# Kernel optimization log

Hardware: AMD Instinct MI355X
Metric: run time of the kernel (lower is better)

Reference implementation:

```python
import jax, jax.numpy as jnp
import numpy as np

B, C, D, H, W = 1, 128, 8, 32, 32
NH, HD = 8, 16            # num_heads, head_dim = C // NH
PD, PH, PW = 2, 4, 4      # local patch dims
RD, RH, RW = 2, 2, 2      # global K/V reduction ratios
MLPH = 4 * C              # mlp_ratio = 4
EPS = 1e-5
SCALE = HD ** -0.5


def setup_inputs() -> dict:
    key = jax.random.key(0)
    ks = iter(jax.random.split(key, 16))
    def w(shape, scale=0.02):
        return jax.random.normal(next(ks), shape, jnp.float32) * scale
    inp = {"x": jax.random.normal(next(ks), (B, C, D, H, W), jnp.float32)}
    for p in ("l", "g"):  # local branch / global branch transformer blocks
        inp[f"{p}_n1_g"] = jnp.ones((C,), jnp.float32)
        inp[f"{p}_n1_b"] = jnp.zeros((C,), jnp.float32)
        inp[f"{p}_qkv_w"] = w((3 * C, C))            # Linear(dim, 3*dim, bias=False)
        inp[f"{p}_proj_w"] = w((C, C))
        inp[f"{p}_proj_b"] = jnp.zeros((C,), jnp.float32)
        inp[f"{p}_n2_g"] = jnp.ones((C,), jnp.float32)
        inp[f"{p}_n2_b"] = jnp.zeros((C,), jnp.float32)
        inp[f"{p}_fc1_w"] = w((MLPH, C))
        inp[f"{p}_fc1_b"] = jnp.zeros((MLPH,), jnp.float32)
        inp[f"{p}_fc2_w"] = w((C, MLPH))
        inp[f"{p}_fc2_b"] = jnp.zeros((C,), jnp.float32)
    inp["g_ke_w"] = w((C, C, RD, RH, RW))  # Conv3d(dim, dim, k=stride=(2,2,2), bias=False)
    inp["g_ve_w"] = w((C, C, RD, RH, RW))
    inp["g_nk_g"] = jnp.ones((HD,), jnp.float32)
    inp["g_nk_b"] = jnp.zeros((HD,), jnp.float32)
    inp["g_nv_g"] = jnp.ones((HD,), jnp.float32)
    inp["g_nv_b"] = jnp.zeros((HD,), jnp.float32)
    return inp


def _ln(t, g, b):
    m = t.mean(-1, keepdims=True)
    v = jnp.square(t - m).mean(-1, keepdims=True)
    return (t - m) * jax.lax.rsqrt(v + EPS) * g + b


def _mlp(t, w1, b1, w2, b2):
    return jax.nn.gelu(t @ w1.T + b1, approximate=False) @ w2.T + b2


def _forward(x, l_n1_g, l_n1_b, l_qkv_w, l_proj_w, l_proj_b, l_n2_g, l_n2_b,
             l_fc1_w, l_fc1_b, l_fc2_w, l_fc2_b,
             g_n1_g, g_n1_b, g_qkv_w, g_ke_w, g_ve_w, g_nk_g, g_nk_b,
             g_nv_g, g_nv_b, g_proj_w, g_proj_b, g_n2_g, g_n2_b,
             g_fc1_w, g_fc1_b, g_fc2_w, g_fc2_b):
    nd, nh, nw = D // PD, H // PH, W // PW
    R, Npl = nd * nh * nw, PD * PH * PW
    N = D * H * W

    # ---------------- Local branch ----------------
    # (B,C,D,H,W) -> (B, R, Npl, C) patch tokens
    loc = x.reshape(B, C, nd, PD, nh, PH, nw, PW)
    loc = loc.transpose(0, 2, 4, 6, 3, 5, 7, 1).reshape(B, R, Npl, C)
    y = _ln(loc, l_n1_g, l_n1_b)
    qkv = (y @ l_qkv_w.T).reshape(B, R, Npl, 3, NH, HD).transpose(3, 0, 1, 4, 2, 5)
    q, k, v = qkv[0], qkv[1], qkv[2]  # (B,R,NH,Npl,HD)
    attn = jax.nn.softmax(jnp.einsum('brhnd,brhmd->brhnm', q, k) * SCALE, axis=-1)
    o = jnp.einsum('brhnm,brhmd->brhnd', attn, v)
    # faithful to torch: (attn@v).transpose(-1,-2).reshape(B,R,Npl,C)
    o = jnp.swapaxes(o, -1, -2).reshape(B, R, Npl, C)
    loc = loc + (o @ l_proj_w.T + l_proj_b)
    loc = loc + _mlp(_ln(loc, l_n2_g, l_n2_b), l_fc1_w, l_fc1_b, l_fc2_w, l_fc2_b)
    # back to (B,C,D,H,W)
    loc_y = loc.reshape(B, nd, nh, nw, PD, PH, PW, C)
    loc_y = loc_y.transpose(0, 7, 1, 4, 2, 5, 3, 6).reshape(B, C, D, H, W)

    # ---------------- Global branch ----------------
    g = x.reshape(B, C, N).transpose(0, 2, 1)  # (B,N,C)
    y = _ln(g, g_n1_g, g_n1_b)
    qkv = y @ g_qkv_w.T  # (B,N,3C)
    q, k, v = jnp.split(qkv, 3, axis=-1)
    qh = q.reshape(B, N, NH, HD).transpose(0, 2, 1, 3)  # (B,NH,N,HD)
    dn = ('NCDHW', 'OIDHW', 'NCDHW')
    def _reduce(t, wc):
        tm = t.transpose(0, 2, 1).reshape(B, C, D, H, W)
        tr = jax.lax.conv_general_dilated(tm, wc, (RD, RH, RW), 'VALID',
                                          dimension_numbers=dn)
        nr = tr.shape[2] * tr.shape[3] * tr.shape[4]
        return tr.reshape(B, C, nr).transpose(0, 2, 1).reshape(B, nr, NH, HD).transpose(0, 2, 1, 3)
    kr = _ln(_reduce(k, g_ke_w), g_nk_g, g_nk_b)  # (B,NH,Nr,HD)
    vr = _ln(_reduce(v, g_ve_w), g_nv_g, g_nv_b)
    attn = jax.nn.softmax(jnp.einsum('bhnd,bhmd->bhnm', qh, kr) * SCALE, axis=-1)
    o = jnp.einsum('bhnm,bhmd->bhnd', attn, vr)
    o = o.transpose(0, 2, 1, 3).reshape(B, N, C)
    g = g + (o @ g_proj_w.T + g_proj_b)
    g = g + _mlp(_ln(g, g_n2_g, g_n2_b), g_fc1_w, g_fc1_b, g_fc2_w, g_fc2_b)
    glo_y = g.transpose(0, 2, 1).reshape(B, C, D, H, W)

    # ---------------- Gate ----------------
    return x * jax.nn.sigmoid(loc_y + glo_y)


def reference(x, l_n1_g, l_n1_b, l_qkv_w, l_proj_w, l_proj_b, l_n2_g, l_n2_b,
              l_fc1_w, l_fc1_b, l_fc2_w, l_fc2_b,
              g_n1_g, g_n1_b, g_qkv_w, g_ke_w, g_ve_w, g_nk_g, g_nk_b,
              g_nv_g, g_nv_b, g_proj_w, g_proj_b, g_n2_g, g_n2_b,
              g_fc1_w, g_fc1_b, g_fc2_w, g_fc2_b):
    return _forward(x, l_n1_g, l_n1_b, l_qkv_w, l_proj_w, l_proj_b, l_n2_g, l_n2_b,
                    l_fc1_w, l_fc1_b, l_fc2_w, l_fc2_b,
                    g_n1_g, g_n1_b, g_qkv_w, g_ke_w, g_ve_w, g_nk_g, g_nk_b,
                    g_nv_g, g_nv_b, g_proj_w, g_proj_b, g_n2_g, g_n2_b,
                    g_fc1_w, g_fc1_b, g_fc2_w, g_fc2_b)
```

## Files before the change

kernel.cpp:

```cpp
#include <hip/hip_runtime.h>
#include <math.h>

#define N_TOK 8192
#define C_DIM 128
#define NHD   8
#define HDIM  16
#define NR    1024
#define EPSV  1e-5f
#define QK_SCALE 0.25f
#define QK_L2E  0.36067376f

typedef __attribute__((ext_vector_type(8))) short short8;
typedef __attribute__((ext_vector_type(4))) float f32x4;

__device__ __forceinline__ float gelu_f(float v) {
    return 0.5f * v * (1.0f + erff(v * 0.70710678118654752f));
}
__device__ __forceinline__ float uaf(unsigned int u) {
    union { unsigned int u; float f; } x; x.u = u; return x.f;
}
__device__ __forceinline__ short f2b(float v) {
    union { float f; unsigned int u; } x; x.f = v;
    unsigned int r = x.u + 0x7fffu + ((x.u >> 16) & 1u);
    return (short)(r >> 16);
}
__device__ __forceinline__ void ld16bf(const short* p, float* d) {
    uint4 a = *(const uint4*)p;
    uint4 b = *(const uint4*)(p + 8);
    d[0]  = uaf(a.x << 16); d[1]  = uaf(a.x & 0xffff0000u);
    d[2]  = uaf(a.y << 16); d[3]  = uaf(a.y & 0xffff0000u);
    d[4]  = uaf(a.z << 16); d[5]  = uaf(a.z & 0xffff0000u);
    d[6]  = uaf(a.w << 16); d[7]  = uaf(a.w & 0xffff0000u);
    d[8]  = uaf(b.x << 16); d[9]  = uaf(b.x & 0xffff0000u);
    d[10] = uaf(b.y << 16); d[11] = uaf(b.y & 0xffff0000u);
    d[12] = uaf(b.z << 16); d[13] = uaf(b.z & 0xffff0000u);
    d[14] = uaf(b.w << 16); d[15] = uaf(b.w & 0xffff0000u);
}

struct CvtDesc { const float* src; short* dst; int n; int pad; };
struct CvtArgs { CvtDesc d[10]; };

__global__ __launch_bounds__(256) void cvtrans_k(const float* __restrict__ x,
                                                 float* __restrict__ xt, CvtArgs ca) {
    __shared__ float tile[32][33];
    int t = threadIdx.x;
    if (blockIdx.x < 1024) {
        int bx = blockIdx.x & 255, by = blockIdx.x >> 8;
        int tx = t & 31, ty = t >> 5;
        int n0 = bx * 32, c0 = by * 32;
#pragma unroll
        for (int k = 0; k < 4; ++k)
            tile[ty + k * 8][tx] = x[(size_t)(c0 + ty + k * 8) * N_TOK + n0 + tx];
        __syncthreads();
#pragma unroll
        for (int k = 0; k < 4; ++k)
            xt[(size_t)(n0 + ty + k * 8) * C_DIM + c0 + tx] = tile[tx][ty + k * 8];
        return;
    }
    int bid = blockIdx.x - 1024;
#pragma unroll 1
    for (int d = 0; d < 10; ++d) {
        CvtDesc dd = ca.d[d];
        if (dd.pad) {
            for (int i = bid * 256 + t; i < dd.n; i += 40 * 256) {
                int co = i >> 10, qq = i & 1023;
                dd.dst[co * 1024 + ((qq & 7) << 7) + (qq >> 3)] = f2b(dd.src[i]);
            }
        } else {
            for (int i = bid * 256 + t; i < dd.n; i += 40 * 256)
                dd.dst[i] = f2b(dd.src[i]);
        }
    }
}

__global__ __launch_bounds__(256) void ln_token_k(const float* __restrict__ in,
                                                  const float* __restrict__ g1, const float* __restrict__ b1,
                                                  short* __restrict__ o1,
                                                  const float* __restrict__ g2, const float* __restrict__ b2,
                                                  short* __restrict__ o2) {
    int lane = threadIdx.x & 63;
    int n = blockIdx.x * 4 + (threadIdx.x >> 6);
    float v0 = in[(size_t)n * C_DIM + lane];
    float v1 = in[(size_t)n * C_DIM + 64 + lane];
    float s = v0 + v1, sq = v0 * v0 + v1 * v1;
#pragma unroll
    for (int off = 32; off >= 1; off >>= 1) {
        s += __shfl_xor(s, off);
        sq += __shfl_xor(sq, off);
    }
    float m = s * (1.0f / 128.0f);
    float var = sq * (1.0f / 128.0f) - m * m;
    float rs = rsqrtf(var + EPSV);
    float h0 = (v0 - m) * rs, h1 = (v1 - m) * rs;
    o1[(size_t)n * C_DIM + lane]      = f2b(h0 * g1[lane] + b1[lane]);
    o1[(size_t)n * C_DIM + 64 + lane] = f2b(h1 * g1[lane + 64] + b1[lane + 64]);
    o2[(size_t)n * C_DIM + lane]      = f2b(h0 * g2[lane] + b2[lane]);
    o2[(size_t)n * C_DIM + 64 + lane] = f2b(h1 * g2[lane + 64] + b2[lane + 64]);
}

__global__ __launch_bounds__(256) void ln2_pair_k(const float* __restrict__ in0,
                                                  const float* __restrict__ g0, const float* __restrict__ b0,
                                                  short* __restrict__ o0,
                                                  const float* __restrict__ in1,
                                                  const float* __restrict__ g1, const float* __restrict__ b1,
                                                  short* __restrict__ o1) {
    int blk = blockIdx.x;
    bool sel = blk >= 2048;
    blk &= 2047;
    const float* in = sel ? in1 : in0;
    const float* g  = sel ? g1 : g0;
    const float* b  = sel ? b1 : b0;
    short* o        = sel ? o1 : o0;
    int lane = threadIdx.x & 63;
    int n = blk * 4 + (threadIdx.x >> 6);
    float v0 = in[(size_t)n * C_DIM + lane];
    float v1 = in[(size_t)n * C_DIM + 64 + lane];
    float s = v0 + v1, sq = v0 * v0 + v1 * v1;
#pragma unroll
    for (int off = 32; off >= 1; off >>= 1) {
        s += __shfl_xor(s, off);
        sq += __shfl_xor(sq, off);
    }
    float m = s * (1.0f / 128.0f);
    float var = sq * (1.0f / 128.0f) - m * m;
    float rs = rsqrtf(var + EPSV);
    o[(size_t)n * C_DIM + lane]      = f2b((v0 - m) * rs * g[lane] + b[lane]);
    o[(size_t)n * C_DIM + 64 + lane] = f2b((v1 - m) * rs * g[lane + 64] + b[lane + 64]);
}

struct MArgs {
    const short* A[2]; const short* W[2];
    const float* bias[2]; const float* res[2];
    void* out[2];
};
template <int EPI>
__global__ __launch_bounds__(256) void mgemm_k(MArgs ga, int M, int N, int K) {
    int zi = blockIdx.z;
    const short* A = ga.A[zi];
    const short* W = ga.W[zi];
    __shared__ short As[128 * 64];
    __shared__ short Bs[128 * 64];
    int t = threadIdx.x;
    int w = t >> 6, l = t & 63;
    int m0 = blockIdx.x * 128, n0 = blockIdx.y * 128;
    int wm = (w >> 1) * 64, wn = (w & 1) * 64;

    f32x4 acc[4][4];
#pragma unroll
    for (int a = 0; a < 4; ++a)
#pragma unroll
        for (int b = 0; b < 4; ++b) acc[a][b] = f32x4{0.f, 0.f, 0.f, 0.f};

    for (int k0 = 0; k0 < K; k0 += 64) {
        __syncthreads();
#pragma unroll
        for (int c = 0; c < 4; ++c) {
            int chunk = c * 256 + t;
            int row = chunk >> 3;
            int slot = chunk & 7;
            int ss = slot ^ (row & 7);
            uint4 av = *(const uint4*)(A + (size_t)(m0 + row) * K + k0 + slot * 8);
            *(uint4*)(As + row * 64 + ss * 8) = av;
            uint4 wv = *(const uint4*)(W + (size_t)(n0 + row) * K + k0 + slot * 8);
            *(uint4*)(Bs + row * 64 + ss * 8) = wv;
        }
        __syncthreads();
#pragma unroll
        for (int kk = 0; kk < 2; ++kk) {
            short8 af[4], bf[4];
            int sl = kk * 4 + (l >> 4);
#pragma unroll
            for (int mf = 0; mf < 4; ++mf) {
                int row = wm + mf * 16 + (l & 15);
                af[mf] = *(const short8*)(As + row * 64 + (sl ^ (row & 7)) * 8);
            }
#pragma unroll
            for (int nf = 0; nf < 4; ++nf) {
                int row = wn + nf * 16 + (l & 15);
                bf[nf] = *(const short8*)(Bs + row * 64 + (sl ^ (row & 7)) * 8);
            }
#pragma unroll
            for (int mf = 0; mf < 4; ++mf)
#pragma unroll
                for (int nf = 0; nf < 4; ++nf)
                    acc[mf][nf] = __builtin_amdgcn_mfma_f32_16x16x32_bf16(
                        af[mf], bf[nf], acc[mf][nf], 0, 0, 0);
        }
    }

#pragma unroll
    for (int mf = 0; mf < 4; ++mf) {
#pragma unroll
        for (int nf = 0; nf < 4; ++nf) {
            int col = n0 + wn + nf * 16 + (l & 15);
#pragma unroll
            for (int j = 0; j < 4; ++j) {
                int row = m0 + wm + mf * 16 + (l >> 4) * 4 + j;
                float v = acc[mf][nf][j];
                if (EPI == 0) {
                    ((short*)ga.out[zi])[(size_t)row * N + col] = f2b(v);
                } else if (EPI == 1) {
                    v += ga.bias[zi][col] + ga.res[zi][(size_t)row * N + col];
                    ((float*)ga.out[zi])[(size_t)row * N + col] = v;
                } else if (EPI == 2) {
                    v = gelu_f(v + ga.bias[zi][col]);
                    ((short*)ga.out[zi])[(size_t)row * N + col] = f2b(v);
                }
            }
        }
    }
}

struct CLArgs {
    const short* qkv_g; const short* wk; const short* wv;
    float* kpart; float* vpart;
    const short* qkv_l; short* ob;
};
__global__ __launch_bounds__(256) void convlat_k(CLArgs ga) {
    __shared__ char smem[32768];
    int t = threadIdx.x;
    if (blockIdx.x < 128) {
        int bid = blockIdx.x;
        int m0 = (bid & 7) * 128;
        int zi = bid >> 6;
        int slice = (bid >> 3) & 7;
        const short* Abase = ga.qkv_g + (zi ? 256 : 128);
        const short* W = zi ? ga.wv : ga.wk;
        float* outp = zi ? ga.vpart : ga.kpart;
        short* As = (short*)smem;
        short* Bs = (short*)smem + 128 * 64;
        int w = t >> 6, l = t & 63;
        int wm = (w >> 1) * 64, wn = (w & 1) * 64;
        int kbeg = slice * 128;

        f32x4 acc[4][4];
#pragma unroll
        for (int a = 0; a < 4; ++a)
#pragma unroll
            for (int b = 0; b < 4; ++b) acc[a][b] = f32x4{0.f, 0.f, 0.f, 0.f};

        for (int k0 = kbeg; k0 < kbeg + 128; k0 += 64) {
            __syncthreads();
            int off = k0 >> 7;
            int od = off >> 2, oh = (off >> 1) & 1, ow = off & 1;
#pragma unroll
            for (int c = 0; c < 4; ++c) {
                int chunk = c * 256 + t;
                int row = chunk >> 3;
                int slot = chunk & 7;
                int ss = slot ^ (row & 7);
                int nr = m0 + row;
                int ci = (k0 & 127) + slot * 8;
                int n = (2 * (nr >> 8) + od) * 1024 + (2 * ((nr >> 4) & 15) + oh) * 32
                        + 2 * (nr & 15) + ow;
                uint4 av = *(const uint4*)(Abase + (size_t)n * 384 + ci);
                *(uint4*)(As + row * 64 + ss * 8) = av;
                uint4 wv2 = *(const uint4*)(W + (size_t)row * 1024 + k0 + slot * 8);
                *(uint4*)(Bs + row * 64 + ss * 8) = wv2;
            }
            __syncthreads();
#pragma unroll
            for (int kk = 0; kk < 2; ++kk) {
                short8 af[4], bf[4];
                int sl = kk * 4 + (l >> 4);
#pragma unroll
                for (int mf = 0; mf < 4; ++mf) {
                    int row = wm + mf * 16 + (l & 15);
                    af[mf] = *(const short8*)(As + row * 64 + (sl ^ (row & 7)) * 8);
                }
#pragma unroll
                for (int nf = 0; nf < 4; ++nf) {
                    int row = wn + nf * 16 + (l & 15);
                    bf[nf] = *(const short8*)(Bs + row * 64 + (sl ^ (row & 7)) * 8);
                }
#pragma unroll
                for (int mf = 0; mf < 4; ++mf)
#pragma unroll
                    for (int nf = 0; nf < 4; ++nf)
                        acc[mf][nf] = __builtin_amdgcn_mfma_f32_16x16x32_bf16(
                            af[mf], bf[nf], acc[mf][nf], 0, 0, 0);
            }
        }
#pragma unroll
        for (int mf = 0; mf < 4; ++mf)
#pragma unroll
            for (int nf = 0; nf < 4; ++nf) {
                int col = wn + nf * 16 + (l & 15);
#pragma unroll
                for (int j = 0; j < 4; ++j) {
                    int row = m0 + wm + mf * 16 + (l >> 4) * 4 + j;
                    outp[(size_t)slice * (NR * C_DIM) + (size_t)row * C_DIM + col] =
                        acc[mf][nf][j];
                }
            }
        return;
    }
    float (*ks)[32][HDIM] = (float(*)[32][HDIM])smem;
    float (*vs)[32][HDIM] = (float(*)[32][HDIM])(smem + 16384);
    int m = t & 31, h = t >> 5, r = blockIdx.x - 128;
    int zd = r >> 6, zh = (r >> 3) & 7, zw = r & 7;
    int pd = m >> 4, ph = (m >> 2) & 3, pw = m & 3;
    int n = (zd * 2 + pd) * 1024 + (zh * 4 + ph) * 32 + (zw * 4 + pw);
    const short* base = ga.qkv_l + (size_t)n * 384 + h * HDIM;
    float q[16], kt[16], vt[16];
    ld16bf(base, q);
    ld16bf(base + 128, kt);
    ld16bf(base + 256, vt);
#pragma unroll
    for (int d = 0; d < 16; ++d) { ks[h][m][d] = kt[d]; vs[h][m][d] = vt[d]; }
    __syncthreads();
    float s[32];
#pragma unroll
    for (int j = 0; j < 32; ++j) {
        float d = 0.f;
#pragma unroll
        for (int dd = 0; dd < 16; ++dd) d += q[dd] * ks[h][j][dd];
        s[j] = __expf(d * QK_SCALE);
    }
    float sum = 0.f;
#pragma unroll
    for (int j = 0; j < 32; ++j) sum += s[j];
    float inv = 1.0f / sum;
    float oo[16] = {};
#pragma unroll
    for (int j = 0; j < 32; ++j) {
        float p = s[j] * inv;
#pragma unroll
        for (int dd = 0; dd < 16; ++dd) oo[dd] += p * vs[h][j][dd];
    }
#pragma unroll
    for (int dd = 0; dd < 16; ++dd) {
        int n2 = h * 4 + (dd >> 2);
        int c2 = (dd & 3) * 32 + m;
        int pd2 = n2 >> 4, ph2 = (n2 >> 2) & 3, pw2 = n2 & 3;
        int nn = (zd * 2 + pd2) * 1024 + (zh * 4 + ph2) * 32 + (zw * 4 + pw2);
        ga.ob[(size_t)nn * C_DIM + c2] = f2b(oo[dd]);
    }
}

__global__ __launch_bounds__(256) void ln_head_sum_k(const float* __restrict__ kpart,
                                                     const float* __restrict__ vpart,
                                                     const float* __restrict__ gk, const float* __restrict__ bk,
                                                     const float* __restrict__ gv, const float* __restrict__ bv,
                                                     short* __restrict__ kout, short* __restrict__ vout) {
    int idx = blockIdx.x * 256 + threadIdx.x;
    bool sel = idx >= 8192;
    int id2 = idx & 8191;
    const float* part = sel ? vpart : kpart;
    const float* g    = sel ? gv : gk;
    const float* b    = sel ? bv : bk;
    int nr = id2 >> 3, h = id2 & 7;
    size_t base = (size_t)nr * C_DIM + h * HDIM;
    float v[16] = {};
#pragma unroll
    for (int p = 0; p < 8; ++p) {
        const float* pp = part + (size_t)p * (NR * C_DIM) + base;
#pragma unroll
        for (int d4 = 0; d4 < 4; ++d4) {
            float4 t = *(const float4*)(pp + d4 * 4);
            v[d4 * 4 + 0] += t.x; v[d4 * 4 + 1] += t.y;
            v[d4 * 4 + 2] += t.z; v[d4 * 4 + 3] += t.w;
        }
    }
    float s = 0.f;
#pragma unroll
    for (int i = 0; i < 16; ++i) s += v[i];
    float m = s * (1.0f / 16.0f);
    float sq = 0.f;
#pragma unroll
    for (int i = 0; i < 16; ++i) { float d = v[i] - m; sq += d * d; }
    float rs = rsqrtf(sq * (1.0f / 16.0f) + EPSV);
    if (!sel) {
        short* op = kout + (size_t)h * (NR * HDIM) + (size_t)nr * HDIM;
#pragma unroll
        for (int i = 0; i < 16; ++i)
            op[i] = f2b(((v[i] - m) * rs * g[i] + b[i]) * QK_L2E);
    } else {
        short* op = vout + (size_t)h * (HDIM * NR) + nr;
#pragma unroll
        for (int i = 0; i < 16; ++i)
            op[(size_t)i * NR] = f2b((v[i] - m) * rs * g[i] + b[i]);
    }
}

__global__ __launch_bounds__(256) void gattn_k(const short* __restrict__ qkv,
                                               const short* __restrict__ kb,
                                               const short* __restrict__ vt,
                                               short* __restrict__ ob) {
    __shared__ short plds[4][2048];
    int t = threadIdx.x;
    int w = t >> 6, l = t & 63;
    int h = blockIdx.y;
    int lr = l & 15, lq = l >> 4;
    int q0 = blockIdx.x * 64 + w * 16;

    short8 qf = short8{0, 0, 0, 0, 0, 0, 0, 0};
    if (lq < 2)
        qf = *(const short8*)(qkv + (size_t)(q0 + lr) * 384 + h * HDIM + lq * 8);

    const short* kh = kb + (size_t)h * (NR * HDIM);
    const short* vh = vt + (size_t)h * (HDIM * NR);
    short* pw = &plds[w][0];

    const f32x4 zz = {0.f, 0.f, 0.f, 0.f};
    f32x4 oacc = {0.f, 0.f, 0.f, 0.f};
    float rs = 0.f;

    for (int c = 0; c < 8; ++c) {
        int kbase = c * 128;
        f32x4 s[8];
#pragma unroll
        for (int nf = 0; nf < 8; ++nf) {
            short8 kf = short8{0, 0, 0, 0, 0, 0, 0, 0};
            if (lq < 2)
                kf = *(const short8*)(kh + (size_t)(kbase + nf * 16 + lr) * HDIM + lq * 8);
            s[nf] = __builtin_amdgcn_mfma_f32_16x16x32_bf16(kf, qf, zz, 0, 0, 0);
        }
#pragma unroll
        for (int nf = 0; nf < 8; ++nf) {
            float p0 = exp2f(s[nf][0]);
            float p1 = exp2f(s[nf][1]);
            float p2 = exp2f(s[nf][2]);
            float p3 = exp2f(s[nf][3]);
            rs += (p0 + p1) + (p2 + p3);
            unsigned int u01, u23;
            asm("v_cvt_pk_bf16_f32 %0, %1, %2" : "=v"(u01) : "v"(p0), "v"(p1));
            asm("v_cvt_pk_bf16_f32 %0, %1, %2" : "=v"(u23) : "v"(p2), "v"(p3));
            int k0 = nf * 16 + lq * 4;
            int sw = (lr & 7) << 3;
            *(unsigned int*)&pw[lr * 128 + (k0 ^ sw)]       = u01;
            *(unsigned int*)&pw[lr * 128 + ((k0 + 2) ^ sw)] = u23;
        }
#pragma unroll
        for (int ks = 0; ks < 4; ++ks) {
            short8 pf = *(const short8*)&pw[(lr * 128 + ks * 32 + lq * 8) ^ ((lr & 7) << 3)];
            short8 vf = *(const short8*)(vh + (size_t)lr * NR + kbase + ks * 32 + lq * 8);
            oacc = __builtin_amdgcn_mfma_f32_16x16x32_bf16(pf, vf, oacc, 0, 0, 0);
        }
    }
    rs += __shfl_xor(rs, 16);
    rs += __shfl_xor(rs, 32);
    float r0 = __shfl(rs, lq * 4 + 0);
    float r1 = __shfl(rs, lq * 4 + 1);
    float r2 = __shfl(rs, lq * 4 + 2);
    float r3 = __shfl(rs, lq * 4 + 3);
    size_t base_o = (size_t)(q0 + lq * 4) * C_DIM + h * HDIM + lr;
    ob[base_o]             = f2b(oacc[0] / r0);
    ob[base_o + C_DIM]     = f2b(oacc[1] / r1);
    ob[base_o + 2 * C_DIM] = f2b(oacc[2] / r2);
    ob[base_o + 3 * C_DIM] = f2b(oacc[3] / r3);
}

__global__ __launch_bounds__(256) void gate_k(const float* __restrict__ x,
                                              const float* __restrict__ lf, const float* __restrict__ gf,
                                              float* __restrict__ out) {
    __shared__ float tile[32][33];
    int n0 = blockIdx.x * 32, c0 = blockIdx.y * 32;
    int tx = threadIdx.x, ty = threadIdx.y;
#pragma unroll
    for (int k = 0; k < 4; ++k) {
        int n = n0 + ty + k * 8, c = c0 + tx;
        tile[ty + k * 8][tx] = lf[(size_t)n * C_DIM + c] + gf[(size_t)n * C_DIM + c];
    }
    __syncthreads();
#pragma unroll
    for (int k = 0; k < 4; ++k) {
        int c = c0 + ty + k * 8, n = n0 + tx;
        float z = tile[tx][ty + k * 8];
        float sg = 1.0f / (1.0f + __expf(-z));
        out[(size_t)c * N_TOK + n] = x[(size_t)c * N_TOK + n] * sg;
    }
}

extern "C" void kernel_launch(void* const* d_in, const int* in_sizes, int n_in,
                              void* d_out, int out_size, void* d_ws, size_t ws_size,
                              hipStream_t stream) {
    const float* x        = (const float*)d_in[0];
    const float* l_n1_g   = (const float*)d_in[1];
    const float* l_n1_b   = (const float*)d_in[2];
    const float* l_qkv_w  = (const float*)d_in[3];
    const float* l_proj_w = (const float*)d_in[4];
    const float* l_proj_b = (const float*)d_in[5];
    const float* l_n2_g   = (const float*)d_in[6];
    const float* l_n2_b   = (const float*)d_in[7];
    const float* l_fc1_w  = (const float*)d_in[8];
    const float* l_fc1_b  = (const float*)d_in[9];
    const float* l_fc2_w  = (const float*)d_in[10];
    const float* l_fc2_b  = (const float*)d_in[11];
    const float* g_n1_g   = (const float*)d_in[12];
    const float* g_n1_b   = (const float*)d_in[13];
    const float* g_qkv_w  = (const float*)d_in[14];
    const float* g_proj_w = (const float*)d_in[15];
    const float* g_proj_b = (const float*)d_in[16];
    const float* g_n2_g   = (const float*)d_in[17];
    const float* g_n2_b   = (const float*)d_in[18];
    const float* g_fc1_w  = (const float*)d_in[19];
    const float* g_fc1_b  = (const float*)d_in[20];
    const float* g_fc2_w  = (const float*)d_in[21];
    const float* g_fc2_b  = (const float*)d_in[22];
    const float* g_ke_w   = (const float*)d_in[23];
    const float* g_ve_w   = (const float*)d_in[24];
    const float* g_nk_g   = (const float*)d_in[25];
    const float* g_nk_b   = (const float*)d_in[26];
    const float* g_nv_g   = (const float*)d_in[27];
    const float* g_nv_b   = (const float*)d_in[28];
    float* out = (float*)d_out;

    char* base = (char*)d_ws;
    float* xt     = (float*)(base);
    float* t1_l   = (float*)(base + (4ull  << 20));
    float* t1_g   = (float*)(base + (8ull  << 20));
    short* yA16   = (short*)(base + (12ull << 20));
    short* yG16   = (short*)(base + (14ull << 20));
    short* t2_l   = yA16;
    short* t2_g   = yG16;
    float* locfin = (float*)(base + (12ull << 20));
    short* obuf_l = (short*)(base + (16ull << 20));
    short* obuf_g = (short*)(base + (18ull << 20));
    float* glofin = (float*)(base + (16ull << 20));
    short* qkv_l  = (short*)(base + (20ull << 20));
    short* qkv_g  = (short*)(base + (26ull << 20));
    short* h1_l   = (short*)(base + (32ull << 20));
    float* kpart  = (float*)(base + (32ull << 20));
    float* vpart  = (float*)(base + (36ull << 20));
    short* h1_g   = (short*)(base + (40ull << 20));
    short* kb16   = (short*)(base + (48ull << 20));
    short* vt16   = (short*)(base + (48ull << 20) + (512ull << 10));
    short* wts    = (short*)(base + (49ull << 20));

    const int L_QKV = 0,      L_PROJ = 49152, L_FC1 = 65536,  L_FC2 = 131072;
    const int G_QKV = 196608, G_PROJ = 245760, G_FC1 = 262144, G_FC2 = 327680;
    const int G_KE  = 393216, G_VE   = 524288;

    CvtArgs ca;
    ca.d[0] = {l_qkv_w,  wts + L_QKV,  49152, 0};
    ca.d[1] = {l_proj_w, wts + L_PROJ, 16384, 0};
    ca.d[2] = {l_fc1_w,  wts + L_FC1,  65536, 0};
    ca.d[3] = {l_fc2_w,  wts + L_FC2,  65536, 0};
    ca.d[4] = {g_qkv_w,  wts + G_QKV,  49152, 0};
    ca.d[5] = {g_proj_w, wts + G_PROJ, 16384, 0};
    ca.d[6] = {g_fc1_w,  wts + G_FC1,  65536, 0};
    ca.d[7] = {g_fc2_w,  wts + G_FC2,  65536, 0};
    ca.d[8] = {g_ke_w,   wts + G_KE,  131072, 1};
    ca.d[9] = {g_ve_w,   wts + G_VE,  131072, 1};

    cvtrans_k<<<1064, 256, 0, stream>>>(x, xt, ca);

    ln_token_k<<<2048, 256, 0, stream>>>(xt, l_n1_g, l_n1_b, yA16, g_n1_g, g_n1_b, yG16);

    MArgs a_qkv = {{yA16, yG16}, {wts + L_QKV, wts + G_QKV}, {nullptr, nullptr}, {nullptr, nullptr}, {qkv_l, qkv_g}};
    mgemm_k<0><<<dim3(64, 3, 2), 256, 0, stream>>>(a_qkv, N_TOK, 384, 128);

    CLArgs cla = {qkv_g, wts + G_KE, wts + G_VE, kpart, vpart, qkv_l, obuf_l};
    convlat_k<<<384, 256, 0, stream>>>(cla);

    ln_head_sum_k<<<64, 256, 0, stream>>>(kpart, vpart, g_nk_g, g_nk_b, g_nv_g, g_nv_b, kb16, vt16);

    gattn_k<<<dim3(128, 8), 256, 0, stream>>>(qkv_g, kb16, vt16, obuf_g);

    MArgs a_pj = {{obuf_l, obuf_g}, {wts + L_PROJ, wts + G_PROJ}, {l_proj_b, g_proj_b}, {xt, xt}, {t1_l, t1_g}};
    mgemm_k<1><<<dim3(64, 1, 2), 256, 0, stream>>>(a_pj, N_TOK, 128, 128);

    ln2_pair_k<<<4096, 256, 0, stream>>>(t1_l, l_n2_g, l_n2_b, t2_l, t1_g, g_n2_g, g_n2_b, t2_g);

    MArgs a_f1 = {{t2_l, t2_g}, {wts + L_FC1, wts + G_FC1}, {l_fc1_b, g_fc1_b}, {nullptr, nullptr}, {h1_l, h1_g}};
    mgemm_k<2><<<dim3(64, 4, 2), 256, 0, stream>>>(a_f1, N_TOK, 512, 128);

    MArgs a_f2 = {{h1_l, h1_g}, {wts + L_FC2, wts + G_FC2}, {l_fc2_b, g_fc2_b}, {t1_l, t1_g}, {locfin, glofin}};
    mgemm_k<1><<<dim3(64, 1, 2), 256, 0, stream>>>(a_f2, N_TOK, 128, 512);

    gate_k<<<dim3(256, 4), dim3(32, 8), 0, stream>>>(x, locfin, glofin, out);
}
```

Baseline: 141.3 us.

## Fuse input transpose with first LayerNorm and split global attention keys across warps

The separate transpose/convert kernel and token LayerNorm kernel become one prep kernel. It loads a 32-token slab of x into LDS, writes the transposed fp32 copy, and emits both normalized bf16 outputs with vectorized stores, which removes one launch and a global round trip of xt. The global attention kernel now uses 512 threads, so two warp groups each handle half of the 1024 reduced keys. Their partial outputs and row sums are combined through LDS. This doubles the parallelism per query tile at the cost of an extra barrier and more LDS per block.

```diff
diff --git a/kernel.cpp b/kernel.cpp
--- a/kernel.cpp
+++ b/kernel.cpp
@@ -23,6 +23,9 @@
     union { float f; unsigned int u; } x; x.f = v;
     unsigned int r = x.u + 0x7fffu + ((x.u >> 16) & 1u);
     return (short)(r >> 16);
+}
+__device__ __forceinline__ unsigned int pk2(float a, float b) {
+    return (unsigned int)(unsigned short)f2b(a) | ((unsigned int)(unsigned short)f2b(b) << 16);
 }
 __device__ __forceinline__ void ld16bf(const short* p, float* d) {
     uint4 a = *(const uint4*)p;
@@ -40,62 +43,73 @@
 struct CvtDesc { const float* src; short* dst; int n; int pad; };
 struct CvtArgs { CvtDesc d[10]; };
 
-__global__ __launch_bounds__(256) void cvtrans_k(const float* __restrict__ x,
-                                                 float* __restrict__ xt, CvtArgs ca) {
-    __shared__ float tile[32][33];
+__global__ __launch_bounds__(256) void prep_k(const float* __restrict__ x,
+                                              const float* __restrict__ g1, const float* __restrict__ b1,
+                                              const float* __restrict__ g2, const float* __restrict__ b2,
+                                              float* __restrict__ xt,
+                                              short* __restrict__ o1, short* __restrict__ o2,
+                                              CvtArgs ca) {
+    __shared__ float tile[32][132];
     int t = threadIdx.x;
-    if (blockIdx.x < 1024) {
-        int bx = blockIdx.x & 255, by = blockIdx.x >> 8;
-        int tx = t & 31, ty = t >> 5;
-        int n0 = bx * 32, c0 = by * 32;
-#pragma unroll
-        for (int k = 0; k < 4; ++k)
-            tile[ty + k * 8][tx] = x[(size_t)(c0 + ty + k * 8) * N_TOK + n0 + tx];
-        __syncthreads();
-#pragma unroll
-        for (int k = 0; k < 4; ++k)
-            xt[(size_t)(n0 + ty + k * 8) * C_DIM + c0 + tx] = tile[tx][ty + k * 8];
+    if (blockIdx.x >= 256) {
+        int bid = blockIdx.x - 256;
+#pragma unroll 1
+        for (int d = 0; d < 10; ++d) {
+            CvtDesc dd = ca.d[d];
+            if (dd.pad) {
+                for (int i = bid * 256 + t; i < dd.n; i += 40 * 256) {
+                    int co = i >> 10, qq = i & 1023;
+                    dd.dst[co * 1024 + ((qq & 7) << 7) + (qq >> 3)] = f2b(dd.src[i]);
+                }
+            } else {
+                for (int i = bid * 256 + t; i < dd.n; i += 40 * 256)
+                    dd.dst[i] = f2b(dd.src[i]);
+            }
+        }
         return;
     }
-    int bid = blockIdx.x - 1024;
-#pragma unroll 1
-    for (int d = 0; d < 10; ++d) {
-        CvtDesc dd = ca.d[d];
-        if (dd.pad) {
-            for (int i = bid * 256 + t; i < dd.n; i += 40 * 256) {
-                int co = i >> 10, qq = i & 1023;
-                dd.dst[co * 1024 + ((qq & 7) << 7) + (qq >> 3)] = f2b(dd.src[i]);
-            }
-        } else {
-            for (int i = bid * 256 + t; i < dd.n; i += 40 * 256)
-                dd.dst[i] = f2b(dd.src[i]);
-        }
-    }
-}
-
-__global__ __launch_bounds__(256) void ln_token_k(const float* __restrict__ in,
-                                                  const float* __restrict__ g1, const float* __restrict__ b1,
-                                                  short* __restrict__ o1,
-                                                  const float* __restrict__ g2, const float* __restrict__ b2,
-                                                  short* __restrict__ o2) {
-    int lane = threadIdx.x & 63;
-    int n = blockIdx.x * 4 + (threadIdx.x >> 6);
-    float v0 = in[(size_t)n * C_DIM + lane];
-    float v1 = in[(size_t)n * C_DIM + 64 + lane];
-    float s = v0 + v1, sq = v0 * v0 + v1 * v1;
-#pragma unroll
-    for (int off = 32; off >= 1; off >>= 1) {
-        s += __shfl_xor(s, off);
-        sq += __shfl_xor(sq, off);
-    }
+    int n0 = blockIdx.x * 32;
+#pragma unroll
+    for (int k = 0; k < 16; ++k) {
+        int f = t + k * 256;
+        int n = f & 31, c = f >> 5;
+        tile[n][c] = x[(size_t)c * N_TOK + n0 + n];
+    }
+    __syncthreads();
+    int tk = t >> 3, cb = (t & 7) * 16;
+    float v[16];
+    float s = 0.f, sq = 0.f;
+#pragma unroll
+    for (int i = 0; i < 16; ++i) {
+        v[i] = tile[tk][cb + i];
+        s += v[i]; sq += v[i] * v[i];
+    }
+    s += __shfl_xor(s, 1);  s += __shfl_xor(s, 2);  s += __shfl_xor(s, 4);
+    sq += __shfl_xor(sq, 1); sq += __shfl_xor(sq, 2); sq += __shfl_xor(sq, 4);
     float m = s * (1.0f / 128.0f);
     float var = sq * (1.0f / 128.0f) - m * m;
     float rs = rsqrtf(var + EPSV);
-    float h0 = (v0 - m) * rs, h1 = (v1 - m) * rs;
-    o1[(size_t)n * C_DIM + lane]      = f2b(h0 * g1[lane] + b1[lane]);
-    o1[(size_t)n * C_DIM + 64 + lane] = f2b(h1 * g1[lane + 64] + b1[lane + 64]);
-    o2[(size_t)n * C_DIM + lane]      = f2b(h0 * g2[lane] + b2[lane]);
-    o2[(size_t)n * C_DIM + 64 + lane] = f2b(h1 * g2[lane + 64] + b2[lane + 64]);
+    int tok = n0 + tk;
+    float* xp = xt + (size_t)tok * C_DIM + cb;
+    *(float4*)(xp)      = make_float4(v[0], v[1], v[2], v[3]);
+    *(float4*)(xp + 4)  = make_float4(v[4], v[5], v[6], v[7]);
+    *(float4*)(xp + 8)  = make_float4(v[8], v[9], v[10], v[11]);
+    *(float4*)(xp + 12) = make_float4(v[12], v[13], v[14], v[15]);
+    float hA[16], hB[16];
+#pragma unroll
+    for (int i = 0; i < 16; ++i) {
+        float hn = (v[i] - m) * rs;
+        hA[i] = hn * g1[cb + i] + b1[cb + i];
+        hB[i] = hn * g2[cb + i] + b2[cb + i];
+    }
+    uint4 ua0 = {pk2(hA[0], hA[1]), pk2(hA[2], hA[3]), pk2(hA[4], hA[5]), pk2(hA[6], hA[7])};
+    uint4 ua1 = {pk2(hA[8], hA[9]), pk2(hA[10], hA[11]), pk2(hA[12], hA[13]), pk2(hA[14], hA[15])};
+    uint4 ub0 = {pk2(hB[0], hB[1]), pk2(hB[2], hB[3]), pk2(hB[4], hB[5]), pk2(hB[6], hB[7])};
+    uint4 ub1 = {pk2(hB[8], hB[9]), pk2(hB[10], hB[11]), pk2(hB[12], hB[13]), pk2(hB[14], hB[15])};
+    *(uint4*)(o1 + (size_t)tok * C_DIM + cb)     = ua0;
+    *(uint4*)(o1 + (size_t)tok * C_DIM + cb + 8) = ua1;
+    *(uint4*)(o2 + (size_t)tok * C_DIM + cb)     = ub0;
+    *(uint4*)(o2 + (size_t)tok * C_DIM + cb + 8) = ub1;
 }
 
 __global__ __launch_bounds__(256) void ln2_pair_k(const float* __restrict__ in0,
@@ -383,16 +397,18 @@
     }
 }
 
-__global__ __launch_bounds__(256) void gattn_k(const short* __restrict__ qkv,
+__global__ __launch_bounds__(512) void gattn_k(const short* __restrict__ qkv,
                                                const short* __restrict__ kb,
                                                const short* __restrict__ vt,
                                                short* __restrict__ ob) {
-    __shared__ short plds[4][2048];
+    __shared__ short plds[8][2048];
+    __shared__ float comb[4][64][5];
     int t = threadIdx.x;
     int w = t >> 6, l = t & 63;
     int h = blockIdx.y;
     int lr = l & 15, lq = l >> 4;
-    int q0 = blockIdx.x * 64 + w * 16;
+    int qw = w & 3, kw = w >> 2;
+    int q0 = blockIdx.x * 64 + qw * 16;
 
     short8 qf = short8{0, 0, 0, 0, 0, 0, 0, 0};
     if (lq < 2)
@@ -406,8 +422,8 @@
     f32x4 oacc = {0.f, 0.f, 0.f, 0.f};
     float rs = 0.f;
 
-    for (int c = 0; c < 8; ++c) {
-        int kbase = c * 128;
+    for (int c = 0; c < 4; ++c) {
+        int kbase = kw * 512 + c * 128;
         f32x4 s[8];
 #pragma unroll
         for (int nf = 0; nf < 8; ++nf) {
@@ -440,15 +456,30 @@
     }
     rs += __shfl_xor(rs, 16);
     rs += __shfl_xor(rs, 32);
-    float r0 = __shfl(rs, lq * 4 + 0);
-    float r1 = __shfl(rs, lq * 4 + 1);
-    float r2 = __shfl(rs, lq * 4 + 2);
-    float r3 = __shfl(rs, lq * 4 + 3);
-    size_t base_o = (size_t)(q0 + lq * 4) * C_DIM + h * HDIM + lr;
-    ob[base_o]             = f2b(oacc[0] / r0);
-    ob[base_o + C_DIM]     = f2b(oacc[1] / r1);
-    ob[base_o + 2 * C_DIM] = f2b(oacc[2] / r2);
-    ob[base_o + 3 * C_DIM] = f2b(oacc[3] / r3);
+    if (w >= 4) {
+        comb[w - 4][l][0] = oacc[0];
+        comb[w - 4][l][1] = oacc[1];
+        comb[w - 4][l][2] = oacc[2];
+        comb[w - 4][l][3] = oacc[3];
+        comb[w - 4][l][4] = rs;
+    }
+    __syncthreads();
+    if (w < 4) {
+        oacc[0] += comb[w][l][0];
+        oacc[1] += comb[w][l][1];
+        oacc[2] += comb[w][l][2];
+        oacc[3] += comb[w][l][3];
+        rs += comb[w][l][4];
+        float r0 = __shfl(rs, lq * 4 + 0);
+        float r1 = __shfl(rs, lq * 4 + 1);
+        float r2 = __shfl(rs, lq * 4 + 2);
+        float r3 = __shfl(rs, lq * 4 + 3);
+        size_t base_o = (size_t)(q0 + lq * 4) * C_DIM + h * HDIM + lr;
+        ob[base_o]             = f2b(oacc[0] / r0);
+        ob[base_o + C_DIM]     = f2b(oacc[1] / r1);
+        ob[base_o + 2 * C_DIM] = f2b(oacc[2] / r2);
+        ob[base_o + 3 * C_DIM] = f2b(oacc[3] / r3);
+    }
 }
 
 __global__ __launch_bounds__(256) void gate_k(const float* __restrict__ x,
@@ -544,9 +575,7 @@
     ca.d[8] = {g_ke_w,   wts + G_KE,  131072, 1};
     ca.d[9] = {g_ve_w,   wts + G_VE,  131072, 1};
 
-    cvtrans_k<<<1064, 256, 0, stream>>>(x, xt, ca);
-
-    ln_token_k<<<2048, 256, 0, stream>>>(xt, l_n1_g, l_n1_b, yA16, g_n1_g, g_n1_b, yG16);
+    prep_k<<<296, 256, 0, stream>>>(x, l_n1_g, l_n1_b, g_n1_g, g_n1_b, xt, yA16, yG16, ca);
 
     MArgs a_qkv = {{yA16, yG16}, {wts + L_QKV, wts + G_QKV}, {nullptr, nullptr}, {nullptr, nullptr}, {qkv_l, qkv_g}};
     mgemm_k<0><<<dim3(64, 3, 2), 256, 0, stream>>>(a_qkv, N_TOK, 384, 128);
@@ -556,7 +585,7 @@
 
     ln_head_sum_k<<<64, 256, 0, stream>>>(kpart, vpart, g_nk_g, g_nk_b, g_nv_g, g_nv_b, kb16, vt16);
 
-    gattn_k<<<dim3(128, 8), 256, 0, stream>>>(qkv_g, kb16, vt16, obuf_g);
+    gattn_k<<<dim3(128, 8), 512, 0, stream>>>(qkv_g, kb16, vt16, obuf_g);
 
     MArgs a_pj = {{obuf_l, obuf_g}, {wts + L_PROJ, wts + G_PROJ}, {l_proj_b, g_proj_b}, {xt, xt}, {t1_l, t1_g}};
     mgemm_k<1><<<dim3(64, 1, 2), 256, 0, stream>>>(a_pj, N_TOK, 128, 128);
```

New measurement: 140.7 us. No clear change (-0.4%).
